# Optimization experiments

Measured on AMD Instinct MI355X. Metric: run time of the kernel, lower is better.

Reference implementation:

```python
import jax, jax.numpy as jnp
import numpy as np

H = 256  # hidden_size


def setup_inputs() -> dict:
    key = jax.random.key(0)
    ks = jax.random.split(key, 9)
    std = 1.0 / np.sqrt(H)
    u = lambda k, shape: jax.random.uniform(k, shape, jnp.float32, -std, std)
    x = jax.random.normal(ks[0], (64, 16, 128, 64), jnp.float32)
    return {
        "x": x,
        "wi0": u(ks[1], (64, 3 * H)),
        "wh0": u(ks[2], (H, 3 * H)),
        "bi0": u(ks[3], (3 * H,)),
        "bh0": u(ks[4], (3 * H,)),
        "wi1": u(ks[5], (H, 3 * H)),
        "wh1": u(ks[6], (H, 3 * H)),
        "bi1": u(ks[7], (3 * H,)),
        "bh1": u(ks[8], (3 * H,)),
    }


def _cell(x_t, h, wi, wh, bi, bh):
    # x_t: (B, N, D), h: (B, N, H). Gates concatenated as [r|z|n].
    gi = x_t @ wi + bi           # (B, N, 3H)
    gh = h @ wh + bh             # (B, N, 3H)
    ir, iz, inn = jnp.split(gi, 3, axis=-1)
    hr, hz, hn = jnp.split(gh, 3, axis=-1)
    r = jax.nn.sigmoid(ir + hr)
    z = jax.nn.sigmoid(iz + hz)
    n = jnp.tanh(inn + r * hn)
    return (1.0 - z) * n + z * h


def reference(x, wi0, wh0, bi0, bh0, wi1, wh1, bi1, bh1):
    seq_len, B, N, _ = x.shape
    h0 = jnp.zeros((B, N, H), x.dtype)
    h1 = jnp.zeros((B, N, H), x.dtype)

    def step(carry, x_t):
        h0, h1 = carry
        h0 = _cell(x_t, h0, wi0, wh0, bi0, bh0)
        h1 = _cell(h0, h1, wi1, wh1, bi1, bh1)
        return (h0, h1), h1

    (h0, h1), output = jax.lax.scan(step, (h0, h1), x)
    hidden_out = jnp.stack([h0, h1], axis=0)  # (num_layers, B, N, H)
    return output, hidden_out
```

## Files before the change

### kernel.cpp

```cpp
#include <hip/hip_runtime.h>


typedef __attribute__((ext_vector_type(8))) __bf16 bf8;
typedef __attribute__((ext_vector_type(8))) unsigned short u16x8;
typedef __attribute__((ext_vector_type(4))) float f32x4;

#define MFMA16(A, B, C) __builtin_amdgcn_mfma_f32_16x16x32_bf16((A), (B), (C), 0, 0, 0)

#define ROWS 2048
#define HID 256
#define NW 768
#define SLOT (ROWS * HID)
#define OUT_HID_OFF ((size_t)64 * ROWS * HID)

#define WI1_OFF 0
#define WH1_OFF 12288

static __device__ __forceinline__ float b2f(unsigned short u) {
  union { unsigned u32; float f; } v;
  v.u32 = ((unsigned)u) << 16;
  return v.f;
}
static __device__ __forceinline__ unsigned short f2b(float f) {
  unsigned u = __float_as_uint(f);
  u += 0x7fffu + ((u >> 16) & 1u);
  return (unsigned short)(u >> 16);
}
static __device__ __forceinline__ float sigm(float x) {
  return 1.0f / (1.0f + __expf(-x));
}
static __device__ __forceinline__ float tanh_fast(float x) {
  x = fminf(15.0f, fmaxf(-15.0f, x));
  float e = __expf(2.0f * x);
  return (e - 1.0f) / (e + 1.0f);
}
static __device__ __forceinline__ float ldin(const void* p, int i, int f32w) {
  return f32w ? ((const float*)p)[i] : b2f(((const unsigned short*)p)[i]);
}
static __device__ __forceinline__ void stout(void* p, size_t i, float v, int f32w) {
  if (f32w) ((float*)p)[i] = v;
  else ((unsigned short*)p)[i] = f2b(v);
}

static __device__ __forceinline__ bf8 ld_h16(const unsigned short* p) {
  union { unsigned long long q[2]; bf8 b; } u;
  u.q[0] = __hip_atomic_load((const unsigned long long*)p, __ATOMIC_RELAXED,
                             __HIP_MEMORY_SCOPE_AGENT);
  u.q[1] = __hip_atomic_load((const unsigned long long*)(p + 4), __ATOMIC_RELAXED,
                             __HIP_MEMORY_SCOPE_AGENT);
  return u.b;
}
static __device__ __forceinline__ void st_h2(unsigned short* p, unsigned short v) {
  asm volatile("global_store_short %0, %1, off sc0 sc1"
               : : "v"(p), "v"((unsigned)v));
}

__global__ void probe_dtype(const unsigned short* x, unsigned* flag) {
  if (blockIdx.x != 0 || threadIdx.x != 0) return;
  int cnt = 0;
  for (int i = 0; i < 256; ++i) {
    float v = b2f(x[i]);
    if (v == v && fabsf(v) <= 8.0f) cnt++;
  }
  *flag = (cnt >= 250) ? 0u : 1u;
}

__global__ void pack_w(const void* __restrict__ W,
                       unsigned short* __restrict__ P, int KK,
                       const unsigned* __restrict__ flag) {
  int i = blockIdx.x * blockDim.x + threadIdx.x;
  int total = 48 * KK * 64;
  if (i >= total) return;
  int f32w = (int)*flag;
  int l = i & 63;
  int kk = (i >> 6) % KK;
  int nb = i / (64 * KK);
  int n = nb * 16 + (l & 15);
  int k0 = kk * 32 + (l >> 4) * 8;
  u16x8 tmp;
#pragma unroll
  for (int e = 0; e < 8; ++e) tmp[e] = f2b(ldin(W, (k0 + e) * NW + n, f32w));
  *(u16x8*)(P + (size_t)i * 8) = tmp;
}

static __device__ __forceinline__ void gemm_x_bf16(
    const unsigned short* aBase, const unsigned short* xw, int lane,
    f32x4* aR, f32x4* aZ, f32x4* aT) {
#pragma unroll
  for (int kk = 0; kk < 2; ++kk) {
    bf8 A0 = *(const bf8*)(aBase + kk * 32);
    bf8 A1 = *(const bf8*)(aBase + 16 * 64 + kk * 32);
    const int lb = lane * 8;
    bf8 Br = *(const bf8*)(xw + 0 * 16384 + kk * 512 + lb);
    bf8 Bz = *(const bf8*)(xw + 1 * 16384 + kk * 512 + lb);
    bf8 Bn = *(const bf8*)(xw + 2 * 16384 + kk * 512 + lb);
    aR[0] = MFMA16(A0, Br, aR[0]);
    aR[1] = MFMA16(A1, Br, aR[1]);
    aZ[0] = MFMA16(A0, Bz, aZ[0]);
    aZ[1] = MFMA16(A1, Bz, aZ[1]);
    aT[0] = MFMA16(A0, Bn, aT[0]);
    aT[1] = MFMA16(A1, Bn, aT[1]);
  }
}
static __device__ __forceinline__ void gemm_x_f32(
    const float* aBase, const unsigned short* xw, int lane,
    f32x4* aR, f32x4* aZ, f32x4* aT) {
#pragma unroll
  for (int kk = 0; kk < 2; ++kk) {
    union { u16x8 u; bf8 b; } A0, A1;
#pragma unroll
    for (int e = 0; e < 8; ++e) {
      A0.u[e] = f2b(aBase[kk * 32 + e]);
      A1.u[e] = f2b(aBase[16 * 64 + kk * 32 + e]);
    }
    const int lb = lane * 8;
    bf8 Br = *(const bf8*)(xw + 0 * 16384 + kk * 512 + lb);
    bf8 Bz = *(const bf8*)(xw + 1 * 16384 + kk * 512 + lb);
    bf8 Bn = *(const bf8*)(xw + 2 * 16384 + kk * 512 + lb);
    aR[0] = MFMA16(A0.b, Br, aR[0]);
    aR[1] = MFMA16(A1.b, Br, aR[1]);
    aZ[0] = MFMA16(A0.b, Bz, aZ[0]);
    aZ[1] = MFMA16(A1.b, Bz, aZ[1]);
    aT[0] = MFMA16(A0.b, Bn, aT[0]);
    aT[1] = MFMA16(A1.b, Bn, aT[1]);
  }
}

__global__ void __launch_bounds__(256, 1) gru_main(
    const void* __restrict__ x,
    const void* __restrict__ bi0, const void* __restrict__ bh0,
    const void* __restrict__ bi1, const void* __restrict__ bh1,
    const unsigned short* __restrict__ pwi0, const unsigned short* __restrict__ pwh0,
    const unsigned short* __restrict__ pwi1, const unsigned short* __restrict__ pwh1,
    void* __restrict__ out,
    unsigned short* __restrict__ h0b, unsigned short* __restrict__ h1b,
    unsigned* __restrict__ flags, const unsigned* __restrict__ flag) {
  __shared__ __align__(16) unsigned short smem[24576];

  const int f32w = (int)*flag;
  const int tid = threadIdx.x;
  const int lane = tid & 63;
  const int wid = tid >> 6;
  const int bid = blockIdx.x;
  const int g = bid & 15;
  const int slice = bid >> 4;

  const int d = slice * 16 + (lane & 15);
  const int rb = g * 128 + wid * 32;
  const int arow = rb + (lane & 15);
  const int koff = (lane >> 4) * 8;
  const int rl = (lane >> 4) * 4;

  unsigned* flagp = flags + (size_t)g * 64;

  for (int i = tid; i < 1536; i += 256) {
    int gg = i >> 9, r = i & 511;
    *(u16x8*)(smem + WI1_OFF + gg * 4096 + r * 8) =
        *(const u16x8*)(pwi1 + (size_t)(gg * 16 + slice) * 4096 + r * 8);
    *(u16x8*)(smem + WH1_OFF + gg * 4096 + r * 8) =
        *(const u16x8*)(pwh1 + (size_t)(gg * 16 + slice) * 4096 + r * 8);
  }
  __syncthreads();

  const unsigned short* xw = pwi0 + (size_t)slice * 1024;
  const unsigned short* w0 = pwh0 + (size_t)slice * 4096;

  const float iR0 = ldin(bi0, d, f32w) + ldin(bh0, d, f32w);
  const float iZ0 = ldin(bi0, 256 + d, f32w) + ldin(bh0, 256 + d, f32w);
  const float iI0 = ldin(bi0, 512 + d, f32w);
  const float iH0 = ldin(bh0, 512 + d, f32w);
  const float iR1 = ldin(bi1, d, f32w) + ldin(bh1, d, f32w);
  const float iZ1 = ldin(bi1, 256 + d, f32w) + ldin(bh1, 256 + d, f32w);
  const float iI1 = ldin(bi1, 512 + d, f32w);
  const float iH1 = ldin(bh1, 512 + d, f32w);

  float h0p[2][4] = {{0, 0, 0, 0}, {0, 0, 0, 0}};
  float h1p[2][4] = {{0, 0, 0, 0}, {0, 0, 0, 0}};

  for (int t = 0; t <= 64; ++t) {
    const int sc = t & 1;
    const int sp = sc ^ 1;

    f32x4 aR0[2], aZ0[2], aI0[2], aH0[2], aR1[2], aZ1[2], aI1[2], aH1[2];
#pragma unroll
    for (int f = 0; f < 2; ++f) {
      aR0[f] = (f32x4){iR0, iR0, iR0, iR0};
      aZ0[f] = (f32x4){iZ0, iZ0, iZ0, iZ0};
      aI0[f] = (f32x4){iI0, iI0, iI0, iI0};
      aH0[f] = (f32x4){iH0, iH0, iH0, iH0};
      aR1[f] = (f32x4){iR1, iR1, iR1, iR1};
      aZ1[f] = (f32x4){iZ1, iZ1, iZ1, iZ1};
      aI1[f] = (f32x4){iI1, iI1, iI1, iI1};
      aH1[f] = (f32x4){iH1, iH1, iH1, iH1};
    }

    if (t < 64) {
      size_t xoff = ((size_t)t * ROWS + arow) * 64 + koff;
      if (f32w) gemm_x_f32((const float*)x + xoff, xw, lane, aR0, aZ0, aI0);
      else gemm_x_bf16((const unsigned short*)x + xoff, xw, lane, aR0, aZ0, aI0);
    }

    if (t > 0) {
      if (lane == 0) {
        const unsigned tgt = 64u * (unsigned)t;
        while (__hip_atomic_load(flagp, __ATOMIC_RELAXED,
                                 __HIP_MEMORY_SCOPE_AGENT) < tgt)
          __builtin_amdgcn_s_sleep(1);
      }
      __builtin_amdgcn_sched_barrier(0);
    }

    const unsigned short* a0b =
        h0b + (size_t)sp * SLOT + (size_t)arow * HID + koff;
    bf8 A00[8], A01[8], A10[8], A11[8];
#pragma unroll
    for (int kk = 0; kk < 8; ++kk) {
      A00[kk] = ld_h16(a0b + kk * 32);
      A01[kk] = ld_h16(a0b + 16 * HID + kk * 32);
    }
    if (t >= 2) {
      const unsigned short* a1b =
          h1b + (size_t)sc * SLOT + (size_t)arow * HID + koff;
#pragma unroll
      for (int kk = 0; kk < 8; ++kk) {
        A10[kk] = ld_h16(a1b + kk * 32);
        A11[kk] = ld_h16(a1b + 16 * HID + kk * 32);
      }
    }

#pragma unroll
    for (int kk = 0; kk < 8; ++kk) {
      const int lb = lane * 8;
      bf8 Br0 = *(const bf8*)(w0 + 0 * 65536 + kk * 512 + lb);
      bf8 Bz0 = *(const bf8*)(w0 + 1 * 65536 + kk * 512 + lb);
      bf8 Bn0 = *(const bf8*)(w0 + 2 * 65536 + kk * 512 + lb);
      bf8 Br1 = *(const bf8*)(smem + WI1_OFF + (0 * 8 + kk) * 512 + lb);
      bf8 Bz1 = *(const bf8*)(smem + WI1_OFF + (1 * 8 + kk) * 512 + lb);
      bf8 Bn1 = *(const bf8*)(smem + WI1_OFF + (2 * 8 + kk) * 512 + lb);
      aR0[0] = MFMA16(A00[kk], Br0, aR0[0]);
      aR0[1] = MFMA16(A01[kk], Br0, aR0[1]);
      aZ0[0] = MFMA16(A00[kk], Bz0, aZ0[0]);
      aZ0[1] = MFMA16(A01[kk], Bz0, aZ0[1]);
      aH0[0] = MFMA16(A00[kk], Bn0, aH0[0]);
      aH0[1] = MFMA16(A01[kk], Bn0, aH0[1]);
      aR1[0] = MFMA16(A00[kk], Br1, aR1[0]);
      aR1[1] = MFMA16(A01[kk], Br1, aR1[1]);
      aZ1[0] = MFMA16(A00[kk], Bz1, aZ1[0]);
      aZ1[1] = MFMA16(A01[kk], Bz1, aZ1[1]);
      aI1[0] = MFMA16(A00[kk], Bn1, aI1[0]);
      aI1[1] = MFMA16(A01[kk], Bn1, aI1[1]);
    }
    if (t >= 2) {
#pragma unroll
      for (int kk = 0; kk < 8; ++kk) {
        const int lb = lane * 8;
        bf8 Br = *(const bf8*)(smem + WH1_OFF + (0 * 8 + kk) * 512 + lb);
        bf8 Bz = *(const bf8*)(smem + WH1_OFF + (1 * 8 + kk) * 512 + lb);
        bf8 Bn = *(const bf8*)(smem + WH1_OFF + (2 * 8 + kk) * 512 + lb);
        aR1[0] = MFMA16(A10[kk], Br, aR1[0]);
        aR1[1] = MFMA16(A11[kk], Br, aR1[1]);
        aZ1[0] = MFMA16(A10[kk], Bz, aZ1[0]);
        aZ1[1] = MFMA16(A11[kk], Bz, aZ1[1]);
        aH1[0] = MFMA16(A10[kk], Bn, aH1[0]);
        aH1[1] = MFMA16(A11[kk], Bn, aH1[1]);
      }
    }

    if (t < 64) {
#pragma unroll
      for (int f = 0; f < 2; ++f) {
#pragma unroll
        for (int j = 0; j < 4; ++j) {
          int row = rb + f * 16 + rl + j;
          float r = sigm(aR0[f][j]);
          float z = sigm(aZ0[f][j]);
          float n = tanh_fast(aI0[f][j] + r * aH0[f][j]);
          float hv = (1.0f - z) * n + z * h0p[f][j];
          h0p[f][j] = hv;
          st_h2(h0b + (size_t)sc * SLOT + (size_t)row * HID + d, f2b(hv));
        }
      }
    }
    if (t >= 1) {
#pragma unroll
      for (int f = 0; f < 2; ++f) {
#pragma unroll
        for (int j = 0; j < 4; ++j) {
          int row = rb + f * 16 + rl + j;
          float r = sigm(aR1[f][j]);
          float z = sigm(aZ1[f][j]);
          float n = tanh_fast(aI1[f][j] + r * aH1[f][j]);
          float hv = (1.0f - z) * n + z * h1p[f][j];
          h1p[f][j] = hv;
          st_h2(h1b + (size_t)sp * SLOT + (size_t)row * HID + d, f2b(hv));
        }
      }
    }

    asm volatile("s_waitcnt vmcnt(0)" ::: "memory");
    if (t < 64 && lane == 0)
      __hip_atomic_fetch_add(flagp, 1u, __ATOMIC_RELAXED,
                             __HIP_MEMORY_SCOPE_AGENT);

    if (t >= 1) {
      const int tm1 = t - 1;
#pragma unroll
      for (int f = 0; f < 2; ++f) {
#pragma unroll
        for (int j = 0; j < 4; ++j) {
          int row = rb + f * 16 + rl + j;
          stout(out, ((size_t)tm1 * ROWS + row) * HID + d, h1p[f][j], f32w);
          if (tm1 == 63)
            stout(out, OUT_HID_OFF + (size_t)SLOT + (size_t)row * HID + d,
                  h1p[f][j], f32w);
        }
      }
    }
    if (t == 63) {
#pragma unroll
      for (int f = 0; f < 2; ++f) {
#pragma unroll
        for (int j = 0; j < 4; ++j) {
          int row = rb + f * 16 + rl + j;
          stout(out, OUT_HID_OFF + (size_t)row * HID + d, h0p[f][j], f32w);
        }
      }
    }
  }
}

extern "C" void kernel_launch(void* const* d_in, const int* in_sizes, int n_in,
                              void* d_out, int out_size, void* d_ws, size_t ws_size,
                              hipStream_t stream) {
  (void)in_sizes; (void)n_in; (void)out_size; (void)ws_size;
  const void* x   = d_in[0];
  const void* wi0 = d_in[1];
  const void* wh0 = d_in[2];
  const void* bi0 = d_in[3];
  const void* bh0 = d_in[4];
  const void* wi1 = d_in[5];
  const void* wh1 = d_in[6];
  const void* bi1 = d_in[7];
  const void* bh1 = d_in[8];
  void* out = d_out;

  char* ws = (char*)d_ws;
  unsigned* flags = (unsigned*)ws;
  unsigned* flag  = (unsigned*)(ws + 4096);
  unsigned short* h0b = (unsigned short*)(ws + 8192);
  unsigned short* h1b = (unsigned short*)(ws + 8192 + 2097152);
  unsigned short* pwi0 = (unsigned short*)(ws + 8192 + 4194304);
  unsigned short* pwh0 = pwi0 + 49152;
  unsigned short* pwi1 = pwh0 + 196608;
  unsigned short* pwh1 = pwi1 + 196608;

  hipMemsetAsync(d_ws, 0, 8192 + 2097152, stream);

  probe_dtype<<<1, 64, 0, stream>>>((const unsigned short*)x, flag);

  pack_w<<<(48 * 2 * 64 + 255) / 256, 256, 0, stream>>>(wi0, pwi0, 2, flag);
  pack_w<<<(48 * 8 * 64 + 255) / 256, 256, 0, stream>>>(wh0, pwh0, 8, flag);
  pack_w<<<(48 * 8 * 64 + 255) / 256, 256, 0, stream>>>(wi1, pwi1, 8, flag);
  pack_w<<<(48 * 8 * 64 + 255) / 256, 256, 0, stream>>>(wh1, pwh1, 8, flag);

  void* kargs[] = {&x, &bi0, &bh0, &bi1, &bh1, &pwi0, &pwh0, &pwi1, &pwh1,
                   &out, &h0b, &h1b, &flags, &flag};
  hipError_t lerr = hipLaunchCooperativeKernel(
      (const void*)gru_main, dim3(256), dim3(256), kargs, 0, stream);
  if (lerr != hipSuccess) {
    (void)hipGetLastError();
    gru_main<<<dim3(256), dim3(256), 0, stream>>>(
        x, bi0, bh0, bi1, bh1, pwi0, pwh0, pwi1, pwh1,
        out, h0b, h1b, flags, flag);
  }
}
```

Before: 854.5 us.

## Repartition GRU blocks to 32-row groups and exchange hidden state via fragment-packed rings

Remaps the 256 blocks from 16 row groups of 128 rows into 64 row groups of 32 rows. Each block's four waves now cover different 16-column slices, so only 4 blocks share a row group and the spin-wait barrier target drops from 64 to 4 arrivals. Hidden state goes through shared memory and is written to global rings already laid out as MFMA A-fragments, with 16-byte atomic stores instead of scattered 2-byte stores. Each block then stages the A operand into LDS with coalesced loads. In exchange, the layer-1 weights are no longer held in LDS and are read from global/L2 each step, and the step gains extra __syncthreads calls.

```diff
diff --git a/kernel.cpp b/kernel.cpp
--- a/kernel.cpp
+++ b/kernel.cpp
@@ -12,9 +12,7 @@
 #define NW 768
 #define SLOT (ROWS * HID)
 #define OUT_HID_OFF ((size_t)64 * ROWS * HID)
-
-#define WI1_OFF 0
-#define WH1_OFF 12288
+#define R0SLOT 524288
 
 static __device__ __forceinline__ float b2f(unsigned short u) {
   union { unsigned u32; float f; } v;
@@ -42,17 +40,21 @@
   else ((unsigned short*)p)[i] = f2b(v);
 }
 
-static __device__ __forceinline__ bf8 ld_h16(const unsigned short* p) {
-  union { unsigned long long q[2]; bf8 b; } u;
+static __device__ __forceinline__ u16x8 ld_h16(const unsigned short* p) {
+  union { unsigned long long q[2]; u16x8 b; } u;
   u.q[0] = __hip_atomic_load((const unsigned long long*)p, __ATOMIC_RELAXED,
                              __HIP_MEMORY_SCOPE_AGENT);
   u.q[1] = __hip_atomic_load((const unsigned long long*)(p + 4), __ATOMIC_RELAXED,
                              __HIP_MEMORY_SCOPE_AGENT);
   return u.b;
 }
-static __device__ __forceinline__ void st_h2(unsigned short* p, unsigned short v) {
-  asm volatile("global_store_short %0, %1, off sc0 sc1"
-               : : "v"(p), "v"((unsigned)v));
+static __device__ __forceinline__ void st_h16(unsigned short* p, u16x8 v) {
+  union { u16x8 s; unsigned long long q[2]; } u;
+  u.s = v;
+  __hip_atomic_store((unsigned long long*)p, u.q[0], __ATOMIC_RELAXED,
+                     __HIP_MEMORY_SCOPE_AGENT);
+  __hip_atomic_store((unsigned long long*)(p + 4), u.q[1], __ATOMIC_RELAXED,
+                     __HIP_MEMORY_SCOPE_AGENT);
 }
 
 __global__ void probe_dtype(const unsigned short* x, unsigned* flag) {
@@ -83,49 +85,6 @@
   *(u16x8*)(P + (size_t)i * 8) = tmp;
 }
 
-static __device__ __forceinline__ void gemm_x_bf16(
-    const unsigned short* aBase, const unsigned short* xw, int lane,
-    f32x4* aR, f32x4* aZ, f32x4* aT) {
-#pragma unroll
-  for (int kk = 0; kk < 2; ++kk) {
-    bf8 A0 = *(const bf8*)(aBase + kk * 32);
-    bf8 A1 = *(const bf8*)(aBase + 16 * 64 + kk * 32);
-    const int lb = lane * 8;
-    bf8 Br = *(const bf8*)(xw + 0 * 16384 + kk * 512 + lb);
-    bf8 Bz = *(const bf8*)(xw + 1 * 16384 + kk * 512 + lb);
-    bf8 Bn = *(const bf8*)(xw + 2 * 16384 + kk * 512 + lb);
-    aR[0] = MFMA16(A0, Br, aR[0]);
-    aR[1] = MFMA16(A1, Br, aR[1]);
-    aZ[0] = MFMA16(A0, Bz, aZ[0]);
-    aZ[1] = MFMA16(A1, Bz, aZ[1]);
-    aT[0] = MFMA16(A0, Bn, aT[0]);
-    aT[1] = MFMA16(A1, Bn, aT[1]);
-  }
-}
-static __device__ __forceinline__ void gemm_x_f32(
-    const float* aBase, const unsigned short* xw, int lane,
-    f32x4* aR, f32x4* aZ, f32x4* aT) {
-#pragma unroll
-  for (int kk = 0; kk < 2; ++kk) {
-    union { u16x8 u; bf8 b; } A0, A1;
-#pragma unroll
-    for (int e = 0; e < 8; ++e) {
-      A0.u[e] = f2b(aBase[kk * 32 + e]);
-      A1.u[e] = f2b(aBase[16 * 64 + kk * 32 + e]);
-    }
-    const int lb = lane * 8;
-    bf8 Br = *(const bf8*)(xw + 0 * 16384 + kk * 512 + lb);
-    bf8 Bz = *(const bf8*)(xw + 1 * 16384 + kk * 512 + lb);
-    bf8 Bn = *(const bf8*)(xw + 2 * 16384 + kk * 512 + lb);
-    aR[0] = MFMA16(A0.b, Br, aR[0]);
-    aR[1] = MFMA16(A1.b, Br, aR[1]);
-    aZ[0] = MFMA16(A0.b, Bz, aZ[0]);
-    aZ[1] = MFMA16(A1.b, Bz, aZ[1]);
-    aT[0] = MFMA16(A0.b, Bn, aT[0]);
-    aT[1] = MFMA16(A1.b, Bn, aT[1]);
-  }
-}
-
 __global__ void __launch_bounds__(256, 1) gru_main(
     const void* __restrict__ x,
     const void* __restrict__ bi0, const void* __restrict__ bh0,
@@ -133,37 +92,33 @@
     const unsigned short* __restrict__ pwi0, const unsigned short* __restrict__ pwh0,
     const unsigned short* __restrict__ pwi1, const unsigned short* __restrict__ pwh1,
     void* __restrict__ out,
-    unsigned short* __restrict__ h0b, unsigned short* __restrict__ h1b,
+    unsigned short* __restrict__ ring0, unsigned short* __restrict__ ring1,
     unsigned* __restrict__ flags, const unsigned* __restrict__ flag) {
-  __shared__ __align__(16) unsigned short smem[24576];
+  __shared__ __align__(16) unsigned short AS[16384];
+  __shared__ __align__(16) unsigned short HS[2][2304];
 
   const int f32w = (int)*flag;
   const int tid = threadIdx.x;
   const int lane = tid & 63;
   const int wid = tid >> 6;
   const int bid = blockIdx.x;
-  const int g = bid & 15;
-  const int slice = bid >> 4;
-
-  const int d = slice * 16 + (lane & 15);
-  const int rb = g * 128 + wid * 32;
+  const int g = bid >> 2;
+  const int slice = bid & 3;
+  const int nb = slice * 4 + wid;
+
+  const int d = nb * 16 + (lane & 15);
+  const int rb = g * 32;
   const int arow = rb + (lane & 15);
   const int koff = (lane >> 4) * 8;
   const int rl = (lane >> 4) * 4;
+  const int cl = wid * 16 + (lane & 15);
 
   unsigned* flagp = flags + (size_t)g * 64;
 
-  for (int i = tid; i < 1536; i += 256) {
-    int gg = i >> 9, r = i & 511;
-    *(u16x8*)(smem + WI1_OFF + gg * 4096 + r * 8) =
-        *(const u16x8*)(pwi1 + (size_t)(gg * 16 + slice) * 4096 + r * 8);
-    *(u16x8*)(smem + WH1_OFF + gg * 4096 + r * 8) =
-        *(const u16x8*)(pwh1 + (size_t)(gg * 16 + slice) * 4096 + r * 8);
-  }
-  __syncthreads();
-
-  const unsigned short* xw = pwi0 + (size_t)slice * 1024;
-  const unsigned short* w0 = pwh0 + (size_t)slice * 4096;
+  const unsigned short* xw  = pwi0 + (size_t)nb * 1024;
+  const unsigned short* w0  = pwh0 + (size_t)nb * 4096;
+  const unsigned short* w1i = pwi1 + (size_t)nb * 4096;
+  const unsigned short* w1h = pwh1 + (size_t)nb * 4096;
 
   const float iR0 = ldin(bi0, d, f32w) + ldin(bh0, d, f32w);
   const float iZ0 = ldin(bi0, 256 + d, f32w) + ldin(bh0, 256 + d, f32w);
@@ -176,6 +131,13 @@
 
   float h0p[2][4] = {{0, 0, 0, 0}, {0, 0, 0, 0}};
   float h1p[2][4] = {{0, 0, 0, 0}, {0, 0, 0, 0}};
+
+  const int ef = tid >> 7;
+  const int ekk = (tid >> 6) & 1;
+  const int eln = tid & 63;
+  const int ehs = (ef * 16 + (eln & 15)) * 72 + ekk * 32 + (eln >> 4) * 8;
+  const size_t ero = (size_t)g * 8192 +
+                     (size_t)(ef * 8 + slice * 2 + ekk) * 512 + eln * 8;
 
   for (int t = 0; t <= 64; ++t) {
     const int sc = t & 1;
@@ -196,73 +158,102 @@
 
     if (t < 64) {
       size_t xoff = ((size_t)t * ROWS + arow) * 64 + koff;
-      if (f32w) gemm_x_f32((const float*)x + xoff, xw, lane, aR0, aZ0, aI0);
-      else gemm_x_bf16((const unsigned short*)x + xoff, xw, lane, aR0, aZ0, aI0);
-    }
-
-    if (t > 0) {
-      if (lane == 0) {
-        const unsigned tgt = 64u * (unsigned)t;
-        while (__hip_atomic_load(flagp, __ATOMIC_RELAXED,
-                                 __HIP_MEMORY_SCOPE_AGENT) < tgt)
-          __builtin_amdgcn_s_sleep(1);
-      }
-      __builtin_amdgcn_sched_barrier(0);
-    }
-
-    const unsigned short* a0b =
-        h0b + (size_t)sp * SLOT + (size_t)arow * HID + koff;
-    bf8 A00[8], A01[8], A10[8], A11[8];
-#pragma unroll
-    for (int kk = 0; kk < 8; ++kk) {
-      A00[kk] = ld_h16(a0b + kk * 32);
-      A01[kk] = ld_h16(a0b + 16 * HID + kk * 32);
-    }
-    if (t >= 2) {
-      const unsigned short* a1b =
-          h1b + (size_t)sc * SLOT + (size_t)arow * HID + koff;
-#pragma unroll
-      for (int kk = 0; kk < 8; ++kk) {
-        A10[kk] = ld_h16(a1b + kk * 32);
-        A11[kk] = ld_h16(a1b + 16 * HID + kk * 32);
-      }
-    }
+#pragma unroll
+      for (int kk = 0; kk < 2; ++kk) {
+        union { u16x8 u; bf8 b; } A0, A1;
+        if (f32w) {
+          const float* ab = (const float*)x + xoff;
+#pragma unroll
+          for (int e = 0; e < 8; ++e) {
+            A0.u[e] = f2b(ab[kk * 32 + e]);
+            A1.u[e] = f2b(ab[16 * 64 + kk * 32 + e]);
+          }
+        } else {
+          const unsigned short* ab = (const unsigned short*)x + xoff;
+          A0.u = *(const u16x8*)(ab + kk * 32);
+          A1.u = *(const u16x8*)(ab + 16 * 64 + kk * 32);
+        }
+        const int lb = lane * 8;
+        bf8 Br = *(const bf8*)(xw + 0 * 16384 + kk * 512 + lb);
+        bf8 Bz = *(const bf8*)(xw + 1 * 16384 + kk * 512 + lb);
+        bf8 Bn = *(const bf8*)(xw + 2 * 16384 + kk * 512 + lb);
+        aR0[0] = MFMA16(A0.b, Br, aR0[0]);
+        aR0[1] = MFMA16(A1.b, Br, aR0[1]);
+        aZ0[0] = MFMA16(A0.b, Bz, aZ0[0]);
+        aZ0[1] = MFMA16(A1.b, Bz, aZ0[1]);
+        aI0[0] = MFMA16(A0.b, Bn, aI0[0]);
+        aI0[1] = MFMA16(A1.b, Bn, aI0[1]);
+      }
+    }
+
+    if (t > 0 && tid == 0) {
+      const unsigned tgt = 4u * (unsigned)t;
+      while (__hip_atomic_load(flagp, __ATOMIC_RELAXED,
+                               __HIP_MEMORY_SCOPE_AGENT) < tgt)
+        __builtin_amdgcn_s_sleep(1);
+    }
+    __syncthreads();
+
+    {
+      const unsigned short* r0 = ring0 + (size_t)sp * R0SLOT + (size_t)g * 8192;
+#pragma unroll
+      for (int i = 0; i < 4; ++i) {
+        int idx = tid + i * 256;
+        int ff = idx >> 6, ln2 = idx & 63;
+        *(u16x8*)(AS + ff * 512 + ln2 * 8) = ld_h16(r0 + ff * 512 + ln2 * 8);
+      }
+      if (t >= 2) {
+        const unsigned short* r1 = ring1 + (size_t)sc * R0SLOT + (size_t)g * 8192;
+#pragma unroll
+        for (int i = 0; i < 4; ++i) {
+          int idx = tid + i * 256;
+          int ff = idx >> 6, ln2 = idx & 63;
+          *(u16x8*)(AS + 8192 + ff * 512 + ln2 * 8) =
+              ld_h16(r1 + ff * 512 + ln2 * 8);
+        }
+      }
+    }
+    __syncthreads();
 
 #pragma unroll
     for (int kk = 0; kk < 8; ++kk) {
       const int lb = lane * 8;
+      bf8 A0 = *(const bf8*)(AS + (0 * 8 + kk) * 512 + lb);
+      bf8 A1 = *(const bf8*)(AS + (1 * 8 + kk) * 512 + lb);
       bf8 Br0 = *(const bf8*)(w0 + 0 * 65536 + kk * 512 + lb);
       bf8 Bz0 = *(const bf8*)(w0 + 1 * 65536 + kk * 512 + lb);
       bf8 Bn0 = *(const bf8*)(w0 + 2 * 65536 + kk * 512 + lb);
-      bf8 Br1 = *(const bf8*)(smem + WI1_OFF + (0 * 8 + kk) * 512 + lb);
-      bf8 Bz1 = *(const bf8*)(smem + WI1_OFF + (1 * 8 + kk) * 512 + lb);
-      bf8 Bn1 = *(const bf8*)(smem + WI1_OFF + (2 * 8 + kk) * 512 + lb);
-      aR0[0] = MFMA16(A00[kk], Br0, aR0[0]);
-      aR0[1] = MFMA16(A01[kk], Br0, aR0[1]);
-      aZ0[0] = MFMA16(A00[kk], Bz0, aZ0[0]);
-      aZ0[1] = MFMA16(A01[kk], Bz0, aZ0[1]);
-      aH0[0] = MFMA16(A00[kk], Bn0, aH0[0]);
-      aH0[1] = MFMA16(A01[kk], Bn0, aH0[1]);
-      aR1[0] = MFMA16(A00[kk], Br1, aR1[0]);
-      aR1[1] = MFMA16(A01[kk], Br1, aR1[1]);
-      aZ1[0] = MFMA16(A00[kk], Bz1, aZ1[0]);
-      aZ1[1] = MFMA16(A01[kk], Bz1, aZ1[1]);
-      aI1[0] = MFMA16(A00[kk], Bn1, aI1[0]);
-      aI1[1] = MFMA16(A01[kk], Bn1, aI1[1]);
+      bf8 Br1 = *(const bf8*)(w1i + 0 * 65536 + kk * 512 + lb);
+      bf8 Bz1 = *(const bf8*)(w1i + 1 * 65536 + kk * 512 + lb);
+      bf8 Bn1 = *(const bf8*)(w1i + 2 * 65536 + kk * 512 + lb);
+      aR0[0] = MFMA16(A0, Br0, aR0[0]);
+      aR0[1] = MFMA16(A1, Br0, aR0[1]);
+      aZ0[0] = MFMA16(A0, Bz0, aZ0[0]);
+      aZ0[1] = MFMA16(A1, Bz0, aZ0[1]);
+      aH0[0] = MFMA16(A0, Bn0, aH0[0]);
+      aH0[1] = MFMA16(A1, Bn0, aH0[1]);
+      aR1[0] = MFMA16(A0, Br1, aR1[0]);
+      aR1[1] = MFMA16(A1, Br1, aR1[1]);
+      aZ1[0] = MFMA16(A0, Bz1, aZ1[0]);
+      aZ1[1] = MFMA16(A1, Bz1, aZ1[1]);
+      aI1[0] = MFMA16(A0, Bn1, aI1[0]);
+      aI1[1] = MFMA16(A1, Bn1, aI1[1]);
     }
     if (t >= 2) {
 #pragma unroll
       for (int kk = 0; kk < 8; ++kk) {
         const int lb = lane * 8;
-        bf8 Br = *(const bf8*)(smem + WH1_OFF + (0 * 8 + kk) * 512 + lb);
-        bf8 Bz = *(const bf8*)(smem + WH1_OFF + (1 * 8 + kk) * 512 + lb);
-        bf8 Bn = *(const bf8*)(smem + WH1_OFF + (2 * 8 + kk) * 512 + lb);
-        aR1[0] = MFMA16(A10[kk], Br, aR1[0]);
-        aR1[1] = MFMA16(A11[kk], Br, aR1[1]);
-        aZ1[0] = MFMA16(A10[kk], Bz, aZ1[0]);
-        aZ1[1] = MFMA16(A11[kk], Bz, aZ1[1]);
-        aH1[0] = MFMA16(A10[kk], Bn, aH1[0]);
-        aH1[1] = MFMA16(A11[kk], Bn, aH1[1]);
+        bf8 A0 = *(const bf8*)(AS + 8192 + (0 * 8 + kk) * 512 + lb);
+        bf8 A1 = *(const bf8*)(AS + 8192 + (1 * 8 + kk) * 512 + lb);
+        bf8 Br = *(const bf8*)(w1h + 0 * 65536 + kk * 512 + lb);
+        bf8 Bz = *(const bf8*)(w1h + 1 * 65536 + kk * 512 + lb);
+        bf8 Bn = *(const bf8*)(w1h + 2 * 65536 + kk * 512 + lb);
+        aR1[0] = MFMA16(A0, Br, aR1[0]);
+        aR1[1] = MFMA16(A1, Br, aR1[1]);
+        aZ1[0] = MFMA16(A0, Bz, aZ1[0]);
+        aZ1[1] = MFMA16(A1, Bz, aZ1[1]);
+        aH1[0] = MFMA16(A0, Bn, aH1[0]);
+        aH1[1] = MFMA16(A1, Bn, aH1[1]);
       }
     }
 
@@ -271,13 +262,12 @@
       for (int f = 0; f < 2; ++f) {
 #pragma unroll
         for (int j = 0; j < 4; ++j) {
-          int row = rb + f * 16 + rl + j;
           float r = sigm(aR0[f][j]);
           float z = sigm(aZ0[f][j]);
           float n = tanh_fast(aI0[f][j] + r * aH0[f][j]);
           float hv = (1.0f - z) * n + z * h0p[f][j];
           h0p[f][j] = hv;
-          st_h2(h0b + (size_t)sc * SLOT + (size_t)row * HID + d, f2b(hv));
+          HS[0][(f * 16 + rl + j) * 72 + cl] = f2b(hv);
         }
       }
     }
@@ -286,19 +276,26 @@
       for (int f = 0; f < 2; ++f) {
 #pragma unroll
         for (int j = 0; j < 4; ++j) {
-          int row = rb + f * 16 + rl + j;
           float r = sigm(aR1[f][j]);
           float z = sigm(aZ1[f][j]);
           float n = tanh_fast(aI1[f][j] + r * aH1[f][j]);
           float hv = (1.0f - z) * n + z * h1p[f][j];
           h1p[f][j] = hv;
-          st_h2(h1b + (size_t)sp * SLOT + (size_t)row * HID + d, f2b(hv));
-        }
-      }
+          HS[1][(f * 16 + rl + j) * 72 + cl] = f2b(hv);
+        }
+      }
+    }
+    __syncthreads();
+
+    if (t < 64) {
+      st_h16(ring0 + (size_t)sc * R0SLOT + ero, *(const u16x8*)(&HS[0][ehs]));
+      if (t >= 1)
+        st_h16(ring1 + (size_t)sp * R0SLOT + ero, *(const u16x8*)(&HS[1][ehs]));
     }
 
     asm volatile("s_waitcnt vmcnt(0)" ::: "memory");
-    if (t < 64 && lane == 0)
+    __syncthreads();
+    if (t < 64 && tid == 0)
       __hip_atomic_fetch_add(flagp, 1u, __ATOMIC_RELAXED,
                              __HIP_MEMORY_SCOPE_AGENT);
 
@@ -346,15 +343,15 @@
 
   char* ws = (char*)d_ws;
   unsigned* flags = (unsigned*)ws;
-  unsigned* flag  = (unsigned*)(ws + 4096);
-  unsigned short* h0b = (unsigned short*)(ws + 8192);
-  unsigned short* h1b = (unsigned short*)(ws + 8192 + 2097152);
-  unsigned short* pwi0 = (unsigned short*)(ws + 8192 + 4194304);
+  unsigned* flag  = (unsigned*)(ws + 16384);
+  unsigned short* ring0 = (unsigned short*)(ws + 32768);
+  unsigned short* ring1 = (unsigned short*)(ws + 32768 + 2097152);
+  unsigned short* pwi0 = (unsigned short*)(ws + 32768 + 4194304);
   unsigned short* pwh0 = pwi0 + 49152;
   unsigned short* pwi1 = pwh0 + 196608;
   unsigned short* pwh1 = pwi1 + 196608;
 
-  hipMemsetAsync(d_ws, 0, 8192 + 2097152, stream);
+  hipMemsetAsync(d_ws, 0, 32768 + 2097152, stream);
 
   probe_dtype<<<1, 64, 0, stream>>>((const unsigned short*)x, flag);
 
@@ -364,13 +361,13 @@
   pack_w<<<(48 * 8 * 64 + 255) / 256, 256, 0, stream>>>(wh1, pwh1, 8, flag);
 
   void* kargs[] = {&x, &bi0, &bh0, &bi1, &bh1, &pwi0, &pwh0, &pwi1, &pwh1,
-                   &out, &h0b, &h1b, &flags, &flag};
+                   &out, &ring0, &ring1, &flags, &flag};
   hipError_t lerr = hipLaunchCooperativeKernel(
       (const void*)gru_main, dim3(256), dim3(256), kargs, 0, stream);
   if (lerr != hipSuccess) {
     (void)hipGetLastError();
     gru_main<<<dim3(256), dim3(256), 0, stream>>>(
         x, bi0, bh0, bi1, bh1, pwi0, pwh0, pwi1, pwh1,
-        out, h0b, h1b, flags, flag);
+        out, ring0, ring1, flags, flag);
   }
 }
```

Result: faster. 733.2 us (-14.2%).

## Specialize warps per GRU layer with separate flags to pipeline layers

Applied to the files above, without the earlier changes.

Splits each block's four waves into two layer-0 waves and two layer-1 waves, each handling 64 rows, with separate per-group progress counters so layer 1 of step t can overlap layer 0 of step t+1. Shared memory now holds wh0 and wi1 while wh1 streams from global. The memset of the h0 buffer is dropped because the t=0 step no longer reads it. This changes the cross-stage schedule and the synchronization pattern, and risks extra flag polling latency and weight-load imbalance between the two wave groups.

```diff
diff --git a/kernel.cpp b/kernel.cpp
--- a/kernel.cpp
+++ b/kernel.cpp
@@ -12,9 +12,6 @@
 #define NW 768
 #define SLOT (ROWS * HID)
 #define OUT_HID_OFF ((size_t)64 * ROWS * HID)
-
-#define WI1_OFF 0
-#define WH1_OFF 12288
 
 static __device__ __forceinline__ float b2f(unsigned short u) {
   union { unsigned u32; float f; } v;
@@ -53,6 +50,10 @@
 static __device__ __forceinline__ void st_h2(unsigned short* p, unsigned short v) {
   asm volatile("global_store_short %0, %1, off sc0 sc1"
                : : "v"(p), "v"((unsigned)v));
+}
+static __device__ __forceinline__ void wait_ge(unsigned* p, unsigned tgt) {
+  while (__hip_atomic_load(p, __ATOMIC_RELAXED, __HIP_MEMORY_SCOPE_AGENT) < tgt)
+    __builtin_amdgcn_s_sleep(1);
 }
 
 __global__ void probe_dtype(const unsigned short* x, unsigned* flag) {
@@ -83,49 +84,6 @@
   *(u16x8*)(P + (size_t)i * 8) = tmp;
 }
 
-static __device__ __forceinline__ void gemm_x_bf16(
-    const unsigned short* aBase, const unsigned short* xw, int lane,
-    f32x4* aR, f32x4* aZ, f32x4* aT) {
-#pragma unroll
-  for (int kk = 0; kk < 2; ++kk) {
-    bf8 A0 = *(const bf8*)(aBase + kk * 32);
-    bf8 A1 = *(const bf8*)(aBase + 16 * 64 + kk * 32);
-    const int lb = lane * 8;
-    bf8 Br = *(const bf8*)(xw + 0 * 16384 + kk * 512 + lb);
-    bf8 Bz = *(const bf8*)(xw + 1 * 16384 + kk * 512 + lb);
-    bf8 Bn = *(const bf8*)(xw + 2 * 16384 + kk * 512 + lb);
-    aR[0] = MFMA16(A0, Br, aR[0]);
-    aR[1] = MFMA16(A1, Br, aR[1]);
-    aZ[0] = MFMA16(A0, Bz, aZ[0]);
-    aZ[1] = MFMA16(A1, Bz, aZ[1]);
-    aT[0] = MFMA16(A0, Bn, aT[0]);
-    aT[1] = MFMA16(A1, Bn, aT[1]);
-  }
-}
-static __device__ __forceinline__ void gemm_x_f32(
-    const float* aBase, const unsigned short* xw, int lane,
-    f32x4* aR, f32x4* aZ, f32x4* aT) {
-#pragma unroll
-  for (int kk = 0; kk < 2; ++kk) {
-    union { u16x8 u; bf8 b; } A0, A1;
-#pragma unroll
-    for (int e = 0; e < 8; ++e) {
-      A0.u[e] = f2b(aBase[kk * 32 + e]);
-      A1.u[e] = f2b(aBase[16 * 64 + kk * 32 + e]);
-    }
-    const int lb = lane * 8;
-    bf8 Br = *(const bf8*)(xw + 0 * 16384 + kk * 512 + lb);
-    bf8 Bz = *(const bf8*)(xw + 1 * 16384 + kk * 512 + lb);
-    bf8 Bn = *(const bf8*)(xw + 2 * 16384 + kk * 512 + lb);
-    aR[0] = MFMA16(A0.b, Br, aR[0]);
-    aR[1] = MFMA16(A1.b, Br, aR[1]);
-    aZ[0] = MFMA16(A0.b, Bz, aZ[0]);
-    aZ[1] = MFMA16(A1.b, Bz, aZ[1]);
-    aT[0] = MFMA16(A0.b, Bn, aT[0]);
-    aT[1] = MFMA16(A1.b, Bn, aT[1]);
-  }
-}
-
 __global__ void __launch_bounds__(256, 1) gru_main(
     const void* __restrict__ x,
     const void* __restrict__ bi0, const void* __restrict__ bh0,
@@ -133,9 +91,9 @@
     const unsigned short* __restrict__ pwi0, const unsigned short* __restrict__ pwh0,
     const unsigned short* __restrict__ pwi1, const unsigned short* __restrict__ pwh1,
     void* __restrict__ out,
-    unsigned short* __restrict__ h0b, unsigned short* __restrict__ h1b,
+    unsigned short* __restrict__ ring0, unsigned short* __restrict__ ring1,
     unsigned* __restrict__ flags, const unsigned* __restrict__ flag) {
-  __shared__ __align__(16) unsigned short smem[24576];
+  __shared__ __align__(16) unsigned short WS[24576];
 
   const int f32w = (int)*flag;
   const int tid = threadIdx.x;
@@ -146,183 +104,190 @@
   const int slice = bid >> 4;
 
   const int d = slice * 16 + (lane & 15);
-  const int rb = g * 128 + wid * 32;
-  const int arow = rb + (lane & 15);
   const int koff = (lane >> 4) * 8;
   const int rl = (lane >> 4) * 4;
 
-  unsigned* flagp = flags + (size_t)g * 64;
+  unsigned* flag0p = flags + (size_t)g * 64;
+  unsigned* flag1p = flag0p + 32;
 
   for (int i = tid; i < 1536; i += 256) {
-    int gg = i >> 9, r = i & 511;
-    *(u16x8*)(smem + WI1_OFF + gg * 4096 + r * 8) =
-        *(const u16x8*)(pwi1 + (size_t)(gg * 16 + slice) * 4096 + r * 8);
-    *(u16x8*)(smem + WH1_OFF + gg * 4096 + r * 8) =
-        *(const u16x8*)(pwh1 + (size_t)(gg * 16 + slice) * 4096 + r * 8);
+    int gk = i >> 6, ln = i & 63;
+    size_t src = (size_t)((gk >> 3) * 16 + slice) * 4096 + (gk & 7) * 512 + ln * 8;
+    *(u16x8*)(WS + gk * 512 + ln * 8) = *(const u16x8*)(pwh0 + src);
+    *(u16x8*)(WS + 12288 + gk * 512 + ln * 8) = *(const u16x8*)(pwi1 + src);
   }
   __syncthreads();
 
-  const unsigned short* xw = pwi0 + (size_t)slice * 1024;
-  const unsigned short* w0 = pwh0 + (size_t)slice * 4096;
-
-  const float iR0 = ldin(bi0, d, f32w) + ldin(bh0, d, f32w);
-  const float iZ0 = ldin(bi0, 256 + d, f32w) + ldin(bh0, 256 + d, f32w);
-  const float iI0 = ldin(bi0, 512 + d, f32w);
-  const float iH0 = ldin(bh0, 512 + d, f32w);
-  const float iR1 = ldin(bi1, d, f32w) + ldin(bh1, d, f32w);
-  const float iZ1 = ldin(bi1, 256 + d, f32w) + ldin(bh1, 256 + d, f32w);
-  const float iI1 = ldin(bi1, 512 + d, f32w);
-  const float iH1 = ldin(bh1, 512 + d, f32w);
-
-  float h0p[2][4] = {{0, 0, 0, 0}, {0, 0, 0, 0}};
-  float h1p[2][4] = {{0, 0, 0, 0}, {0, 0, 0, 0}};
-
-  for (int t = 0; t <= 64; ++t) {
-    const int sc = t & 1;
-    const int sp = sc ^ 1;
-
-    f32x4 aR0[2], aZ0[2], aI0[2], aH0[2], aR1[2], aZ1[2], aI1[2], aH1[2];
-#pragma unroll
-    for (int f = 0; f < 2; ++f) {
-      aR0[f] = (f32x4){iR0, iR0, iR0, iR0};
-      aZ0[f] = (f32x4){iZ0, iZ0, iZ0, iZ0};
-      aI0[f] = (f32x4){iI0, iI0, iI0, iI0};
-      aH0[f] = (f32x4){iH0, iH0, iH0, iH0};
-      aR1[f] = (f32x4){iR1, iR1, iR1, iR1};
-      aZ1[f] = (f32x4){iZ1, iZ1, iZ1, iZ1};
-      aI1[f] = (f32x4){iI1, iI1, iI1, iI1};
-      aH1[f] = (f32x4){iH1, iH1, iH1, iH1};
-    }
-
-    if (t < 64) {
-      size_t xoff = ((size_t)t * ROWS + arow) * 64 + koff;
-      if (f32w) gemm_x_f32((const float*)x + xoff, xw, lane, aR0, aZ0, aI0);
-      else gemm_x_bf16((const unsigned short*)x + xoff, xw, lane, aR0, aZ0, aI0);
-    }
-
-    if (t > 0) {
-      if (lane == 0) {
-        const unsigned tgt = 64u * (unsigned)t;
-        while (__hip_atomic_load(flagp, __ATOMIC_RELAXED,
-                                 __HIP_MEMORY_SCOPE_AGENT) < tgt)
-          __builtin_amdgcn_s_sleep(1);
-      }
-      __builtin_amdgcn_sched_barrier(0);
-    }
-
-    const unsigned short* a0b =
-        h0b + (size_t)sp * SLOT + (size_t)arow * HID + koff;
-    bf8 A00[8], A01[8], A10[8], A11[8];
-#pragma unroll
-    for (int kk = 0; kk < 8; ++kk) {
-      A00[kk] = ld_h16(a0b + kk * 32);
-      A01[kk] = ld_h16(a0b + 16 * HID + kk * 32);
-    }
-    if (t >= 2) {
-      const unsigned short* a1b =
-          h1b + (size_t)sc * SLOT + (size_t)arow * HID + koff;
-#pragma unroll
-      for (int kk = 0; kk < 8; ++kk) {
-        A10[kk] = ld_h16(a1b + kk * 32);
-        A11[kk] = ld_h16(a1b + 16 * HID + kk * 32);
-      }
-    }
-
-#pragma unroll
-    for (int kk = 0; kk < 8; ++kk) {
-      const int lb = lane * 8;
-      bf8 Br0 = *(const bf8*)(w0 + 0 * 65536 + kk * 512 + lb);
-      bf8 Bz0 = *(const bf8*)(w0 + 1 * 65536 + kk * 512 + lb);
-      bf8 Bn0 = *(const bf8*)(w0 + 2 * 65536 + kk * 512 + lb);
-      bf8 Br1 = *(const bf8*)(smem + WI1_OFF + (0 * 8 + kk) * 512 + lb);
-      bf8 Bz1 = *(const bf8*)(smem + WI1_OFF + (1 * 8 + kk) * 512 + lb);
-      bf8 Bn1 = *(const bf8*)(smem + WI1_OFF + (2 * 8 + kk) * 512 + lb);
-      aR0[0] = MFMA16(A00[kk], Br0, aR0[0]);
-      aR0[1] = MFMA16(A01[kk], Br0, aR0[1]);
-      aZ0[0] = MFMA16(A00[kk], Bz0, aZ0[0]);
-      aZ0[1] = MFMA16(A01[kk], Bz0, aZ0[1]);
-      aH0[0] = MFMA16(A00[kk], Bn0, aH0[0]);
-      aH0[1] = MFMA16(A01[kk], Bn0, aH0[1]);
-      aR1[0] = MFMA16(A00[kk], Br1, aR1[0]);
-      aR1[1] = MFMA16(A01[kk], Br1, aR1[1]);
-      aZ1[0] = MFMA16(A00[kk], Bz1, aZ1[0]);
-      aZ1[1] = MFMA16(A01[kk], Bz1, aZ1[1]);
-      aI1[0] = MFMA16(A00[kk], Bn1, aI1[0]);
-      aI1[1] = MFMA16(A01[kk], Bn1, aI1[1]);
-    }
-    if (t >= 2) {
-#pragma unroll
-      for (int kk = 0; kk < 8; ++kk) {
+  if (wid < 2) {
+    const int wrb = g * 128 + wid * 64;
+    const unsigned short* xw = pwi0 + (size_t)slice * 1024;
+    const float iR0 = ldin(bi0, d, f32w) + ldin(bh0, d, f32w);
+    const float iZ0 = ldin(bi0, 256 + d, f32w) + ldin(bh0, 256 + d, f32w);
+    const float iI0 = ldin(bi0, 512 + d, f32w);
+    const float iH0 = ldin(bh0, 512 + d, f32w);
+    float h0p[4][4] = {{0}};
+
+    for (int t = 0; t < 64; ++t) {
+      const int sc = t & 1, sp = sc ^ 1;
+      f32x4 aR[4], aZ[4], aI[4], aH[4];
+#pragma unroll
+      for (int f = 0; f < 4; ++f) {
+        aR[f] = (f32x4){iR0, iR0, iR0, iR0};
+        aZ[f] = (f32x4){iZ0, iZ0, iZ0, iZ0};
+        aI[f] = (f32x4){iI0, iI0, iI0, iI0};
+        aH[f] = (f32x4){iH0, iH0, iH0, iH0};
+      }
+#pragma unroll
+      for (int kk = 0; kk < 2; ++kk) {
         const int lb = lane * 8;
-        bf8 Br = *(const bf8*)(smem + WH1_OFF + (0 * 8 + kk) * 512 + lb);
-        bf8 Bz = *(const bf8*)(smem + WH1_OFF + (1 * 8 + kk) * 512 + lb);
-        bf8 Bn = *(const bf8*)(smem + WH1_OFF + (2 * 8 + kk) * 512 + lb);
-        aR1[0] = MFMA16(A10[kk], Br, aR1[0]);
-        aR1[1] = MFMA16(A11[kk], Br, aR1[1]);
-        aZ1[0] = MFMA16(A10[kk], Bz, aZ1[0]);
-        aZ1[1] = MFMA16(A11[kk], Bz, aZ1[1]);
-        aH1[0] = MFMA16(A10[kk], Bn, aH1[0]);
-        aH1[1] = MFMA16(A11[kk], Bn, aH1[1]);
-      }
-    }
-
-    if (t < 64) {
-#pragma unroll
-      for (int f = 0; f < 2; ++f) {
+        bf8 Br = *(const bf8*)(xw + 0 * 16384 + kk * 512 + lb);
+        bf8 Bz = *(const bf8*)(xw + 1 * 16384 + kk * 512 + lb);
+        bf8 Bn = *(const bf8*)(xw + 2 * 16384 + kk * 512 + lb);
+#pragma unroll
+        for (int f = 0; f < 4; ++f) {
+          int row = wrb + f * 16 + (lane & 15);
+          size_t xo = ((size_t)t * ROWS + row) * 64 + kk * 32 + koff;
+          union { u16x8 u; bf8 b; } A;
+          if (f32w) {
+            const float* ab = (const float*)x + xo;
+#pragma unroll
+            for (int e = 0; e < 8; ++e) A.u[e] = f2b(ab[e]);
+          } else {
+            A.u = *(const u16x8*)((const unsigned short*)x + xo);
+          }
+          aR[f] = MFMA16(A.b, Br, aR[f]);
+          aZ[f] = MFMA16(A.b, Bz, aZ[f]);
+          aI[f] = MFMA16(A.b, Bn, aI[f]);
+        }
+      }
+      if (t >= 1) {
+        if (lane == 0) {
+          wait_ge(flag0p, 32u * (unsigned)t);
+          if (t >= 2) wait_ge(flag1p, 32u * (unsigned)(t - 1));
+        }
+        __builtin_amdgcn_sched_barrier(0);
+        const unsigned short* r0 = ring0 + (size_t)sp * SLOT;
+#pragma unroll
+        for (int kk = 0; kk < 8; ++kk) {
+          const int lb = lane * 8;
+          bf8 Br = *(const bf8*)(WS + (0 * 8 + kk) * 512 + lb);
+          bf8 Bz = *(const bf8*)(WS + (1 * 8 + kk) * 512 + lb);
+          bf8 Bn = *(const bf8*)(WS + (2 * 8 + kk) * 512 + lb);
+#pragma unroll
+          for (int f = 0; f < 4; ++f) {
+            int row = wrb + f * 16 + (lane & 15);
+            bf8 A = ld_h16(r0 + (size_t)row * HID + kk * 32 + koff);
+            aR[f] = MFMA16(A, Br, aR[f]);
+            aZ[f] = MFMA16(A, Bz, aZ[f]);
+            aH[f] = MFMA16(A, Bn, aH[f]);
+          }
+        }
+      }
+#pragma unroll
+      for (int f = 0; f < 4; ++f) {
 #pragma unroll
         for (int j = 0; j < 4; ++j) {
-          int row = rb + f * 16 + rl + j;
-          float r = sigm(aR0[f][j]);
-          float z = sigm(aZ0[f][j]);
-          float n = tanh_fast(aI0[f][j] + r * aH0[f][j]);
+          int row = wrb + f * 16 + rl + j;
+          float r = sigm(aR[f][j]);
+          float z = sigm(aZ[f][j]);
+          float n = tanh_fast(aI[f][j] + r * aH[f][j]);
           float hv = (1.0f - z) * n + z * h0p[f][j];
           h0p[f][j] = hv;
-          st_h2(h0b + (size_t)sc * SLOT + (size_t)row * HID + d, f2b(hv));
-        }
-      }
+          st_h2(ring0 + (size_t)sc * SLOT + (size_t)row * HID + d, f2b(hv));
+          if (t == 63) stout(out, OUT_HID_OFF + (size_t)row * HID + d, hv, f32w);
+        }
+      }
+      asm volatile("s_waitcnt vmcnt(0)" ::: "memory");
+      if (lane == 0)
+        __hip_atomic_fetch_add(flag0p, 1u, __ATOMIC_RELAXED,
+                               __HIP_MEMORY_SCOPE_AGENT);
     }
-    if (t >= 1) {
-#pragma unroll
-      for (int f = 0; f < 2; ++f) {
+  } else {
+    const int wrb = g * 128 + (wid - 2) * 64;
+    const unsigned short* w1h = pwh1 + (size_t)slice * 4096;
+    const float iR1 = ldin(bi1, d, f32w) + ldin(bh1, d, f32w);
+    const float iZ1 = ldin(bi1, 256 + d, f32w) + ldin(bh1, 256 + d, f32w);
+    const float iI1 = ldin(bi1, 512 + d, f32w);
+    const float iH1 = ldin(bh1, 512 + d, f32w);
+    float h1p[4][4] = {{0}};
+
+    for (int t = 0; t < 64; ++t) {
+      const int sc = t & 1, sp = sc ^ 1;
+      f32x4 aR[4], aZ[4], aI[4], aH[4];
+#pragma unroll
+      for (int f = 0; f < 4; ++f) {
+        aR[f] = (f32x4){iR1, iR1, iR1, iR1};
+        aZ[f] = (f32x4){iZ1, iZ1, iZ1, iZ1};
+        aI[f] = (f32x4){iI1, iI1, iI1, iI1};
+        aH[f] = (f32x4){iH1, iH1, iH1, iH1};
+      }
+      if (lane == 0) {
+        wait_ge(flag0p, 32u * (unsigned)(t + 1));
+        if (t >= 1) wait_ge(flag1p, 32u * (unsigned)t);
+      }
+      __builtin_amdgcn_sched_barrier(0);
+      {
+        const unsigned short* r0 = ring0 + (size_t)sc * SLOT;
+#pragma unroll
+        for (int kk = 0; kk < 8; ++kk) {
+          const int lb = lane * 8;
+          bf8 Br = *(const bf8*)(WS + 12288 + (0 * 8 + kk) * 512 + lb);
+          bf8 Bz = *(const bf8*)(WS + 12288 + (1 * 8 + kk) * 512 + lb);
+          bf8 Bn = *(const bf8*)(WS + 12288 + (2 * 8 + kk) * 512 + lb);
+#pragma unroll
+          for (int f = 0; f < 4; ++f) {
+            int row = wrb + f * 16 + (lane & 15);
+            bf8 A = ld_h16(r0 + (size_t)row * HID + kk * 32 + koff);
+            aR[f] = MFMA16(A, Br, aR[f]);
+            aZ[f] = MFMA16(A, Bz, aZ[f]);
+            aI[f] = MFMA16(A, Bn, aI[f]);
+          }
+        }
+      }
+      if (t >= 1) {
+        const unsigned short* r1 = ring1 + (size_t)sp * SLOT;
+#pragma unroll
+        for (int kk = 0; kk < 8; ++kk) {
+          const int lb = lane * 8;
+          bf8 Br = *(const bf8*)(w1h + 0 * 65536 + kk * 512 + lb);
+          bf8 Bz = *(const bf8*)(w1h + 1 * 65536 + kk * 512 + lb);
+          bf8 Bn = *(const bf8*)(w1h + 2 * 65536 + kk * 512 + lb);
+#pragma unroll
+          for (int f = 0; f < 4; ++f) {
+            int row = wrb + f * 16 + (lane & 15);
+            bf8 A = ld_h16(r1 + (size_t)row * HID + kk * 32 + koff);
+            aR[f] = MFMA16(A, Br, aR[f]);
+            aZ[f] = MFMA16(A, Bz, aZ[f]);
+            aH[f] = MFMA16(A, Bn, aH[f]);
+          }
+        }
+      }
+#pragma unroll
+      for (int f = 0; f < 4; ++f) {
 #pragma unroll
         for (int j = 0; j < 4; ++j) {
-          int row = rb + f * 16 + rl + j;
-          float r = sigm(aR1[f][j]);
-          float z = sigm(aZ1[f][j]);
-          float n = tanh_fast(aI1[f][j] + r * aH1[f][j]);
+          int row = wrb + f * 16 + rl + j;
+          float r = sigm(aR[f][j]);
+          float z = sigm(aZ[f][j]);
+          float n = tanh_fast(aI[f][j] + r * aH[f][j]);
           float hv = (1.0f - z) * n + z * h1p[f][j];
           h1p[f][j] = hv;
-          st_h2(h1b + (size_t)sp * SLOT + (size_t)row * HID + d, f2b(hv));
-        }
-      }
-    }
-
-    asm volatile("s_waitcnt vmcnt(0)" ::: "memory");
-    if (t < 64 && lane == 0)
-      __hip_atomic_fetch_add(flagp, 1u, __ATOMIC_RELAXED,
-                             __HIP_MEMORY_SCOPE_AGENT);
-
-    if (t >= 1) {
-      const int tm1 = t - 1;
-#pragma unroll
-      for (int f = 0; f < 2; ++f) {
+          st_h2(ring1 + (size_t)sc * SLOT + (size_t)row * HID + d, f2b(hv));
+        }
+      }
+      asm volatile("s_waitcnt vmcnt(0)" ::: "memory");
+      if (lane == 0)
+        __hip_atomic_fetch_add(flag1p, 1u, __ATOMIC_RELAXED,
+                               __HIP_MEMORY_SCOPE_AGENT);
+#pragma unroll
+      for (int f = 0; f < 4; ++f) {
 #pragma unroll
         for (int j = 0; j < 4; ++j) {
-          int row = rb + f * 16 + rl + j;
-          stout(out, ((size_t)tm1 * ROWS + row) * HID + d, h1p[f][j], f32w);
-          if (tm1 == 63)
+          int row = wrb + f * 16 + rl + j;
+          stout(out, ((size_t)t * ROWS + row) * HID + d, h1p[f][j], f32w);
+          if (t == 63)
             stout(out, OUT_HID_OFF + (size_t)SLOT + (size_t)row * HID + d,
                   h1p[f][j], f32w);
-        }
-      }
-    }
-    if (t == 63) {
-#pragma unroll
-      for (int f = 0; f < 2; ++f) {
-#pragma unroll
-        for (int j = 0; j < 4; ++j) {
-          int row = rb + f * 16 + rl + j;
-          stout(out, OUT_HID_OFF + (size_t)row * HID + d, h0p[f][j], f32w);
         }
       }
     }
@@ -347,14 +312,14 @@
   char* ws = (char*)d_ws;
   unsigned* flags = (unsigned*)ws;
   unsigned* flag  = (unsigned*)(ws + 4096);
-  unsigned short* h0b = (unsigned short*)(ws + 8192);
-  unsigned short* h1b = (unsigned short*)(ws + 8192 + 2097152);
+  unsigned short* ring0 = (unsigned short*)(ws + 8192);
+  unsigned short* ring1 = (unsigned short*)(ws + 8192 + 2097152);
   unsigned short* pwi0 = (unsigned short*)(ws + 8192 + 4194304);
   unsigned short* pwh0 = pwi0 + 49152;
   unsigned short* pwi1 = pwh0 + 196608;
   unsigned short* pwh1 = pwi1 + 196608;
 
-  hipMemsetAsync(d_ws, 0, 8192 + 2097152, stream);
+  hipMemsetAsync(d_ws, 0, 8192, stream);
 
   probe_dtype<<<1, 64, 0, stream>>>((const unsigned short*)x, flag);
 
@@ -364,13 +329,13 @@
   pack_w<<<(48 * 8 * 64 + 255) / 256, 256, 0, stream>>>(wh1, pwh1, 8, flag);
 
   void* kargs[] = {&x, &bi0, &bh0, &bi1, &bh1, &pwi0, &pwh0, &pwi1, &pwh1,
-                   &out, &h0b, &h1b, &flags, &flag};
+                   &out, &ring0, &ring1, &flags, &flag};
   hipError_t lerr = hipLaunchCooperativeKernel(
       (const void*)gru_main, dim3(256), dim3(256), kargs, 0, stream);
   if (lerr != hipSuccess) {
     (void)hipGetLastError();
     gru_main<<<dim3(256), dim3(256), 0, stream>>>(
         x, bi0, bh0, bi1, bh1, pwi0, pwh0, pwi1, pwh1,
-        out, h0b, h1b, flags, flag);
+        out, ring0, ring1, flags, flag);
   }
 }
```

Result: slower. 1.402 ms (+64.0%).
